# Performance work log

Measured on AMD Instinct MI355X. Metric: run time of the kernel, lower is better.

## Reference

```python
import jax, jax.numpy as jnp
import numpy as np

B, C, H, W = 4, 64, 64, 64
C8 = C // 8


def setup_inputs() -> dict:
    key = jax.random.key(0)
    ks = jax.random.split(key, 8)
    s = 1.0 / np.sqrt(C)
    return {
        "x": jax.random.normal(ks[0], (B, C, H, W), dtype=jnp.float32),
        "Wq": jax.random.normal(ks[1], (C8, C), dtype=jnp.float32) * s,
        "bq": jnp.zeros((C8,), dtype=jnp.float32),
        "Wk": jax.random.normal(ks[2], (C8, C), dtype=jnp.float32) * s,
        "bk": jnp.zeros((C8,), dtype=jnp.float32),
        "Wv": jax.random.normal(ks[3], (C, C), dtype=jnp.float32) * s,
        "bv": jnp.zeros((C,), dtype=jnp.float32),
        "gamma": jnp.zeros((1,), dtype=jnp.float32),
    }


def reference(x, Wq, bq, Wk, bk, Wv, bv, gamma):
    b, c, h, w = x.shape
    hw = h * w
    xf = x.reshape(b, c, hw)  # [B, C, HW]
    # 1x1 convs == per-pixel linear projections
    q = jnp.einsum("dc,bcn->bnd", Wq, xf) + bq            # [B, HW, C/8]
    k = jnp.einsum("dc,bcn->bdn", Wk, xf) + bk[:, None]   # [B, C/8, HW]
    v = jnp.einsum("dc,bcn->bdn", Wv, xf) + bv[:, None]   # [B, C, HW]
    scale = 1.0 / jnp.sqrt(jnp.asarray(c // 8, dtype=x.dtype))
    attn = jax.nn.softmax(jnp.einsum("bnd,bdm->bnm", q, k) * scale, axis=-1)  # [B, HW, HW]
    # out[:, :, n] = sum_m attn[n, m] * v[:, :, m]
    out = jnp.einsum("bnm,bcm->bcn", attn, v).reshape(b, c, h, w)
    return gamma[0] * out + x
```

## Files before the change

### kernel.cpp

```cpp
#include <hip/hip_runtime.h>

#define HW 4096

typedef float f32x4 __attribute__((ext_vector_type(4)));
typedef __bf16 bf16x8 __attribute__((ext_vector_type(8)));
typedef unsigned short u16x8 __attribute__((ext_vector_type(8)));

union F8 { bf16x8 v; unsigned long long q[2]; unsigned short u[8]; __bf16 h[8]; };

__device__ inline unsigned short f2bf(float f) {
    unsigned int u = __builtin_bit_cast(unsigned int, f);
    u += 0x7fffu + ((u >> 16) & 1u);
    return (unsigned short)(u >> 16);
}
__device__ inline float bf2f(unsigned short h) {
    unsigned int u = ((unsigned int)h) << 16;
    return __builtin_bit_cast(float, u);
}
__device__ inline bf16x8 frag_lo(const unsigned short* p) {
    F8 f; f.q[0] = *(const unsigned long long*)p; f.q[1] = 0ull; return f.v;
}

#define MFMA16(a,b,c) __builtin_amdgcn_mfma_f32_16x16x32_bf16(a, b, c, 0, 0, 0)
#define EXP2(x) __builtin_amdgcn_exp2f(x)

__global__ __launch_bounds__(256, 4) void proj_kernel(
    const float* __restrict__ x,
    const float* __restrict__ Wq, const float* __restrict__ bq,
    const float* __restrict__ Wk, const float* __restrict__ bk,
    const float* __restrict__ Wv, const float* __restrict__ bv,
    unsigned short* __restrict__ qpack, unsigned short* __restrict__ kpack,
    unsigned short* __restrict__ vt3)
{
    const float A2 = 0.51006977f;
    __shared__ float ldsW[80][64];
    __shared__ float ldsB[80];

    const int blk   = blockIdx.x;
    const int b     = blk >> 8;
    const int rest  = blk & 255;
    const int ntile = rest >> 2;
    const int rg    = rest & 3;
    const int tid   = threadIdx.x;
    const int w     = tid >> 6;
    const int lane  = tid & 63;
    const int n     = ntile * 64 + lane;

#pragma unroll
    for (int kk = 0; kk < 5; ++kk) {
        const int idx = tid + kk * 256;
        const int r   = idx >> 4;
        const int c   = (idx & 15) << 2;
        f32x4 val;
        if (r < 8) { val = *(const f32x4*)(Wq + r * 64 + c); val *= A2; }
        else if (r < 16) val = *(const f32x4*)(Wk + (r - 8) * 64 + c);
        else             val = *(const f32x4*)(Wv + (r - 16) * 64 + c);
        *(f32x4*)(&ldsW[r][c]) = val;
    }
    if (tid < 80) {
        float bb = (tid < 8) ? bq[tid] * A2
                 : (tid < 16) ? bk[tid - 8] : bv[tid - 16];
        ldsB[tid] = bb;
    }
    __syncthreads();

    const float* xb = x + (size_t)b * 64 * HW + n;
    float xv[64];
#pragma unroll
    for (int c = 0; c < 64; ++c) xv[c] = xb[c * HW];

    auto rowdot = [&](int row) -> float {
        const float* wr = &ldsW[row][0];
        float a0 = 0.f, a1 = 0.f, a2 = 0.f, a3 = 0.f;
#pragma unroll
        for (int c4 = 0; c4 < 16; ++c4) {
            f32x4 wv = *(const f32x4*)(wr + c4 * 4);
            a0 = fmaf(wv[0], xv[c4*4+0], a0);
            a1 = fmaf(wv[1], xv[c4*4+1], a1);
            a2 = fmaf(wv[2], xv[c4*4+2], a2);
            a3 = fmaf(wv[3], xv[c4*4+3], a3);
        }
        return (a0 + a1) + (a2 + a3) + ldsB[row];
    };

    const int vslot = (((n >> 2) & 3) << 3) + (n & 3) + (((n >> 4) & 1) << 2);
    unsigned short* vB = vt3 + ((size_t)(b * 128 + (n >> 5)) * 64) * 32 + vslot;

    const int r0 = rg * 20 + w * 5;
#pragma unroll
    for (int rr = 0; rr < 5; ++rr) {
        const int row = r0 + rr;
        float val = rowdot(row);
        if (row < 8) {
            qpack[(size_t)(b * HW + n) * 8 + row] = f2bf(val);
        } else if (row < 16) {
            kpack[(size_t)(b * HW + n) * 8 + (row - 8)] = f2bf(val);
        } else {
            vB[(size_t)(row - 16) * 32] = f2bf(val);
        }
    }
}

__global__ __launch_bounds__(512, 2) void attn_kernel(
    const unsigned short* __restrict__ qpack,
    const unsigned short* __restrict__ kpack,
    const unsigned short* __restrict__ vt3,
    const float* __restrict__ x,
    const float* __restrict__ gamma,
    float* __restrict__ out)
{
    const int blk  = blockIdx.x;
    const int slot = blk & 7;
    const int j8   = blk >> 3;
    const int b    = slot >> 1;
    const int qt   = (j8 << 1) | (slot & 1);
    const int nb   = qt * 32;
    const int tid  = threadIdx.x;
    const int w    = tid >> 6;
    const int lane = tid & 63;
    const int g    = lane >> 4;
    const int ln   = lane & 15;

    __shared__ unsigned short ldsO[8][32][66];
    __shared__ float ldsL[8][32];

    F8 zf; zf.q[0] = 0ull; zf.q[1] = 0ull;

    bf16x8 qf[2];
#pragma unroll
    for (int i = 0; i < 2; ++i)
        qf[i] = (g == 0)
              ? frag_lo(qpack + (size_t)(b * HW + nb + 16 * i + ln) * 8)
              : zf.v;

    F8 onesu;
#pragma unroll
    for (int e = 0; e < 8; ++e) onesu.u[e] = 0x3F80;
    const bf16x8 ones = onesu.v;

    f32x4 o[2][4], ol[2];
#pragma unroll
    for (int i = 0; i < 2; ++i) {
#pragma unroll
        for (int j = 0; j < 4; ++j) o[i][j] = (f32x4){0,0,0,0};
        ol[i] = (f32x4){0,0,0,0};
    }

    const int mq = w * 512;
    const unsigned short* kb = kpack + (size_t)(b * HW + mq + ln) * 8;
    const unsigned short* vwin = vt3 + ((size_t)b * 128 + w * 16) * 2048
                               + ln * 32 + 8 * g;

#pragma unroll 2
    for (int ch = 0; ch < 16; ++ch) {
        const unsigned short* kp = kb + ch * 256;
        bf16x8 kf0 = (g == 0) ? frag_lo(kp)       : zf.v;
        bf16x8 kf1 = (g == 0) ? frag_lo(kp + 128) : zf.v;
        const unsigned short* vp = vwin + ch * 2048;
        bf16x8 vf0 = *(const bf16x8*)(vp);
        bf16x8 vf1 = *(const bf16x8*)(vp + 512);
        bf16x8 vf2 = *(const bf16x8*)(vp + 1024);
        bf16x8 vf3 = *(const bf16x8*)(vp + 1536);

        const f32x4 z = {0.f, 0.f, 0.f, 0.f};
#pragma unroll
        for (int i = 0; i < 2; ++i) {
            f32x4 s0 = MFMA16(kf0, qf[i], z);
            f32x4 s1 = MFMA16(kf1, qf[i], z);
            F8 pa;
#pragma unroll
            for (int r = 0; r < 4; ++r) {
                pa.h[r]     = (__bf16)EXP2(s0[r]);
                pa.h[r + 4] = (__bf16)EXP2(s1[r]);
            }
            __builtin_amdgcn_s_setprio(1);
            o[i][0] = MFMA16(pa.v, vf0, o[i][0]);
            o[i][1] = MFMA16(pa.v, vf1, o[i][1]);
            o[i][2] = MFMA16(pa.v, vf2, o[i][2]);
            o[i][3] = MFMA16(pa.v, vf3, o[i][3]);
            ol[i]   = MFMA16(pa.v, ones, ol[i]);
            __builtin_amdgcn_s_setprio(0);
        }
    }

#pragma unroll
    for (int i = 0; i < 2; ++i) {
#pragma unroll
        for (int r = 0; r < 4; ++r) {
#pragma unroll
            for (int j = 0; j < 4; ++j)
                ldsO[w][16 * i + 4 * g + r][16 * j + ln] = f2bf(o[i][j][r]);
        }
    }
    if (ln == 0) {
#pragma unroll
        for (int i = 0; i < 2; ++i)
#pragma unroll
            for (int r = 0; r < 4; ++r)
                ldsL[w][16 * i + 4 * g + r] = ol[i][r];
    }
    __syncthreads();

    const int q  = tid & 31;
    const int cc = tid >> 5;
    float L = 0.f;
#pragma unroll
    for (int wv = 0; wv < 8; ++wv) L += ldsL[wv][q];
    const float inv = 1.0f / L;
    const float gm  = gamma[0];
#pragma unroll
    for (int j = 0; j < 4; ++j) {
        const int c = cc + 16 * j;
        float Ov = 0.f;
#pragma unroll
        for (int wv = 0; wv < 8; ++wv) Ov += bf2f(ldsO[wv][q][c]);
        const size_t idx = (size_t)(b * 64 + c) * HW + nb + q;
        out[idx] = fmaf(gm, Ov * inv, x[idx]);
    }
}

extern "C" void kernel_launch(void* const* d_in, const int* in_sizes, int n_in,
                              void* d_out, int out_size, void* d_ws, size_t ws_size,
                              hipStream_t stream) {
    const float* x  = (const float*)d_in[0];
    const float* Wq = (const float*)d_in[1];
    const float* bq = (const float*)d_in[2];
    const float* Wk = (const float*)d_in[3];
    const float* bk = (const float*)d_in[4];
    const float* Wv = (const float*)d_in[5];
    const float* bv = (const float*)d_in[6];
    const float* gm = (const float*)d_in[7];

    unsigned short* qpack = (unsigned short*)d_ws;
    unsigned short* kpack = qpack + 4 * HW * 8;
    unsigned short* vt3   = kpack + 4 * HW * 8;
    float* out = (float*)d_out;

    proj_kernel<<<1024, 256, 0, stream>>>(x, Wq, bq, Wk, bk, Wv, bv,
                                          qpack, kpack, vt3);
    attn_kernel<<<512, 512, 0, stream>>>(qpack, kpack, vt3, x, gm, out);
}
```

Baseline: 33.89 us.

## Double query tile per attention block to 64 and halve grid

Each attention block now handles 64 queries instead of 32, so every K/V fragment loaded from global memory is reused across four query sub-tiles. The grid is halved to 256 blocks, launch bounds drop to one block per CU, and the s_setprio hints around the PV MFMAs are removed. The cross-wave reduction now has waves 4-7 accumulate into waves 0-3's LDS slots, adding a second sync and an extra bf16 rounding. The trade-off is higher register pressure and fewer blocks (256, roughly one per CU) to hide latency.

After: 31.82 us. 6.1% less time.

```diff
diff --git a/kernel.cpp b/kernel.cpp
--- a/kernel.cpp
+++ b/kernel.cpp
@@ -4,7 +4,6 @@
 
 typedef float f32x4 __attribute__((ext_vector_type(4)));
 typedef __bf16 bf16x8 __attribute__((ext_vector_type(8)));
-typedef unsigned short u16x8 __attribute__((ext_vector_type(8)));
 
 union F8 { bf16x8 v; unsigned long long q[2]; unsigned short u[8]; __bf16 h[8]; };
 
@@ -101,7 +100,7 @@
     }
 }
 
-__global__ __launch_bounds__(512, 2) void attn_kernel(
+__global__ __launch_bounds__(512, 1) void attn_kernel(
     const unsigned short* __restrict__ qpack,
     const unsigned short* __restrict__ kpack,
     const unsigned short* __restrict__ vt3,
@@ -111,24 +110,24 @@
 {
     const int blk  = blockIdx.x;
     const int slot = blk & 7;
-    const int j8   = blk >> 3;
+    const int j32  = blk >> 3;
     const int b    = slot >> 1;
-    const int qt   = (j8 << 1) | (slot & 1);
-    const int nb   = qt * 32;
+    const int qt   = (j32 << 1) | (slot & 1);
+    const int nb   = qt * 64;
     const int tid  = threadIdx.x;
     const int w    = tid >> 6;
     const int lane = tid & 63;
     const int g    = lane >> 4;
     const int ln   = lane & 15;
 
-    __shared__ unsigned short ldsO[8][32][66];
-    __shared__ float ldsL[8][32];
+    __shared__ unsigned short ldsO[4][64][66];
+    __shared__ float ldsL[8][64];
 
     F8 zf; zf.q[0] = 0ull; zf.q[1] = 0ull;
 
-    bf16x8 qf[2];
-#pragma unroll
-    for (int i = 0; i < 2; ++i)
+    bf16x8 qf[4];
+#pragma unroll
+    for (int i = 0; i < 4; ++i)
         qf[i] = (g == 0)
               ? frag_lo(qpack + (size_t)(b * HW + nb + 16 * i + ln) * 8)
               : zf.v;
@@ -138,9 +137,9 @@
     for (int e = 0; e < 8; ++e) onesu.u[e] = 0x3F80;
     const bf16x8 ones = onesu.v;
 
-    f32x4 o[2][4], ol[2];
-#pragma unroll
-    for (int i = 0; i < 2; ++i) {
+    f32x4 o[4][4], ol[4];
+#pragma unroll
+    for (int i = 0; i < 4; ++i) {
 #pragma unroll
         for (int j = 0; j < 4; ++j) o[i][j] = (f32x4){0,0,0,0};
         ol[i] = (f32x4){0,0,0,0};
@@ -156,7 +155,7 @@
         const unsigned short* kp = kb + ch * 256;
         bf16x8 kf0 = (g == 0) ? frag_lo(kp)       : zf.v;
         bf16x8 kf1 = (g == 0) ? frag_lo(kp + 128) : zf.v;
-        const unsigned short* vp = vwin + ch * 2048;
+        const unsigned short* vp = vwin + (size_t)ch * 2048;
         bf16x8 vf0 = *(const bf16x8*)(vp);
         bf16x8 vf1 = *(const bf16x8*)(vp + 512);
         bf16x8 vf2 = *(const bf16x8*)(vp + 1024);
@@ -164,7 +163,7 @@
 
         const f32x4 z = {0.f, 0.f, 0.f, 0.f};
 #pragma unroll
-        for (int i = 0; i < 2; ++i) {
+        for (int i = 0; i < 4; ++i) {
             f32x4 s0 = MFMA16(kf0, qf[i], z);
             f32x4 s1 = MFMA16(kf1, qf[i], z);
             F8 pa;
@@ -173,47 +172,57 @@
                 pa.h[r]     = (__bf16)EXP2(s0[r]);
                 pa.h[r + 4] = (__bf16)EXP2(s1[r]);
             }
-            __builtin_amdgcn_s_setprio(1);
             o[i][0] = MFMA16(pa.v, vf0, o[i][0]);
             o[i][1] = MFMA16(pa.v, vf1, o[i][1]);
             o[i][2] = MFMA16(pa.v, vf2, o[i][2]);
             o[i][3] = MFMA16(pa.v, vf3, o[i][3]);
             ol[i]   = MFMA16(pa.v, ones, ol[i]);
-            __builtin_amdgcn_s_setprio(0);
         }
     }
 
-#pragma unroll
-    for (int i = 0; i < 2; ++i) {
-#pragma unroll
-        for (int r = 0; r < 4; ++r) {
-#pragma unroll
-            for (int j = 0; j < 4; ++j)
-                ldsO[w][16 * i + 4 * g + r][16 * j + ln] = f2bf(o[i][j][r]);
-        }
+    if (w < 4) {
+#pragma unroll
+        for (int i = 0; i < 4; ++i)
+#pragma unroll
+            for (int r = 0; r < 4; ++r)
+#pragma unroll
+                for (int j = 0; j < 4; ++j)
+                    ldsO[w][16 * i + 4 * g + r][16 * j + ln] = f2bf(o[i][j][r]);
     }
     if (ln == 0) {
 #pragma unroll
-        for (int i = 0; i < 2; ++i)
+        for (int i = 0; i < 4; ++i)
 #pragma unroll
             for (int r = 0; r < 4; ++r)
                 ldsL[w][16 * i + 4 * g + r] = ol[i][r];
     }
     __syncthreads();
-
-    const int q  = tid & 31;
-    const int cc = tid >> 5;
+    if (w >= 4) {
+        const int s = w - 4;
+#pragma unroll
+        for (int i = 0; i < 4; ++i)
+#pragma unroll
+            for (int r = 0; r < 4; ++r)
+#pragma unroll
+                for (int j = 0; j < 4; ++j) {
+                    unsigned short* p = &ldsO[s][16 * i + 4 * g + r][16 * j + ln];
+                    *p = f2bf(bf2f(*p) + o[i][j][r]);
+                }
+    }
+    __syncthreads();
+
+    const int q  = tid & 63;
+    const int cg = tid >> 6;
     float L = 0.f;
 #pragma unroll
     for (int wv = 0; wv < 8; ++wv) L += ldsL[wv][q];
     const float inv = 1.0f / L;
     const float gm  = gamma[0];
 #pragma unroll
-    for (int j = 0; j < 4; ++j) {
-        const int c = cc + 16 * j;
-        float Ov = 0.f;
-#pragma unroll
-        for (int wv = 0; wv < 8; ++wv) Ov += bf2f(ldsO[wv][q][c]);
+    for (int jj = 0; jj < 8; ++jj) {
+        const int c = cg + 8 * jj;
+        float Ov = bf2f(ldsO[0][q][c]) + bf2f(ldsO[1][q][c])
+                 + bf2f(ldsO[2][q][c]) + bf2f(ldsO[3][q][c]);
         const size_t idx = (size_t)(b * 64 + c) * HW + nb + q;
         out[idx] = fmaf(gm, Ov * inv, x[idx]);
     }
@@ -238,5 +247,5 @@
 
     proj_kernel<<<1024, 256, 0, stream>>>(x, Wq, bq, Wk, bk, Wv, bv,
                                           qpack, kpack, vt3);
-    attn_kernel<<<512, 512, 0, stream>>>(qpack, kpack, vt3, x, gm, out);
-}
+    attn_kernel<<<256, 512, 0, stream>>>(qpack, kpack, vt3, x, gm, out);
+}
```
